# Optimization experiments

Hardware: AMD Instinct MI355X
Metric: run time of the kernel (lower is better)

Reference implementation:

```python
import jax, jax.numpy as jnp
import numpy as np

N_NODES = 50000
N_EDGES = 800000
D_IN = 128
D_OUT = 128


def setup_inputs() -> dict:
    key = jax.random.key(0)
    k1, k2, k3, k4 = jax.random.split(key, 4)
    input_feature = jax.random.normal(k1, (N_NODES, D_IN), dtype=jnp.float32)
    # COO sparse adjacency: edge_index[0]=row (dst), edge_index[1]=col (src)
    edge_index = jax.random.randint(k2, (2, N_EDGES), 0, N_NODES, dtype=jnp.int32)
    edge_weight = jax.random.uniform(k3, (N_EDGES,), dtype=jnp.float32)
    # kaiming-uniform-like init for weight; zeros bias (as in reset_parameters)
    bound = float(np.sqrt(6.0 / D_IN))
    weight = jax.random.uniform(k4, (D_IN, D_OUT), dtype=jnp.float32, minval=-bound, maxval=bound)
    bias = jnp.zeros((D_OUT,), dtype=jnp.float32)
    return {
        "input_feature": input_feature,
        "edge_index": edge_index,
        "edge_weight": edge_weight,
        "weight": weight,
        "bias": bias,
    }


def reference(input_feature, edge_index, edge_weight, weight, bias):
    # support = X @ W  -> [N, D_OUT]
    support = input_feature @ weight
    # sparse A @ support via gather + weighted segment_sum over destination rows
    row, col = edge_index[0], edge_index[1]
    msgs = support[col] * edge_weight[:, None]          # [E, D_OUT]
    output = jax.ops.segment_sum(msgs, row, num_segments=N_NODES)
    return output + bias
```

## Files before the change

### kernel.cpp

```cpp
#include <hip/hip_runtime.h>


#define N_NODES 50000
#define N_EDGES 800000
#define D 128
#define BROWS 66
#define NBUCKET 758
#define SLOT 1536
#define CHUNK 2048
#define EPT 8
#define GEMM_BLOCKS 782
#define PASS1_BLOCKS 391
#define CSTRIDE 16

typedef short bf16x8 __attribute__((ext_vector_type(8)));
typedef float f32x4 __attribute__((ext_vector_type(4)));

__device__ inline unsigned short f2bf(float f) {
    unsigned u = __float_as_uint(f);
    unsigned r = (u + 0x7FFFu + ((u >> 16) & 1u)) >> 16;
    return (unsigned short)r;
}


__global__ __launch_bounds__(256) void wprep_kernel(const float* __restrict__ W,
                                                    unsigned short* __restrict__ WT,
                                                    int* __restrict__ gcursor) {
    int idx = blockIdx.x * 256 + threadIdx.x;
    if (idx < 128 * 128) {
        int k = idx >> 7, n = idx & 127;
        WT[n * 136 + k] = f2bf(W[idx]);
    }
    if (idx < NBUCKET * CSTRIDE) gcursor[idx] = 0;
}

__global__ __launch_bounds__(256) void fused_kernel(const float* __restrict__ X,
                                                    const unsigned short* __restrict__ WT,
                                                    unsigned short* __restrict__ S16,
                                                    const int* __restrict__ ei,
                                                    const float* __restrict__ ew,
                                                    int* __restrict__ gcursor,
                                                    int2* __restrict__ staging) {
    __shared__ __align__(16) char shmem[29712];
    const int t = threadIdx.x;
    const int lane = t & 63, wid = t >> 6;

    if (blockIdx.x < GEMM_BLOCKS) {
        unsigned short* xt = (unsigned short*)shmem;
        const int row0 = blockIdx.x * 64;

        const float4* X4 = (const float4*)X;
#pragma unroll
        for (int i = 0; i < 8; ++i) {
            int idx4 = t + 256 * i;
            int r = idx4 >> 5, c4 = idx4 & 31;
            int gr = row0 + r;
            float4 v = make_float4(0.f, 0.f, 0.f, 0.f);
            if (gr < N_NODES) v = X4[gr * 32 + c4];
            ushort4 u = make_ushort4(f2bf(v.x), f2bf(v.y), f2bf(v.z), f2bf(v.w));
            *(ushort4*)&xt[r * 136 + c4 * 4] = u;
        }
        __syncthreads();

        const int m = lane & 15;
        const int q = lane >> 4;
        const int rbase = wid * 16;

        f32x4 acc[8];
#pragma unroll
        for (int nt = 0; nt < 8; ++nt) acc[nt] = (f32x4){0.f, 0.f, 0.f, 0.f};
#pragma unroll
        for (int ks = 0; ks < 4; ++ks) {
            bf16x8 a = *(const bf16x8*)&xt[(rbase + m) * 136 + ks * 32 + q * 8];
#pragma unroll
            for (int nt = 0; nt < 8; ++nt) {
                bf16x8 b = *(const bf16x8*)&WT[(nt * 16 + m) * 136 + ks * 32 + q * 8];
                acc[nt] = __builtin_amdgcn_mfma_f32_16x16x32_bf16(a, b, acc[nt], 0, 0, 0);
            }
        }
        __syncthreads();
#pragma unroll
        for (int nt = 0; nt < 8; ++nt) {
            int col = nt * 16 + m;
#pragma unroll
            for (int r = 0; r < 4; ++r) {
                int rl = rbase + q * 4 + r;
                xt[rl * 136 + col] = f2bf(acc[nt][r]);
            }
        }
        __syncthreads();
#pragma unroll
        for (int i = 0; i < 4; ++i) {
            int id = t + 256 * i;
            int r = id >> 4, c8 = (id & 15) * 8;
            int gr = row0 + r;
            if (gr < N_NODES)
                *(uint4*)&S16[gr * 128 + c8] = *(const uint4*)&xt[r * 136 + c8];
        }
    } else {
        int* bufx            = (int*)shmem;
        int* bufw            = (int*)(shmem + 8192);
        unsigned short* bof  = (unsigned short*)(shmem + 16384);
        int* hist            = (int*)(shmem + 20480);
        int* lcur            = (int*)(shmem + 23552);
        int* bmg             = (int*)(shmem + 26624);
        int* wsum            = (int*)(shmem + 29696);
        const int base = (blockIdx.x - GEMM_BLOCKS) * CHUNK;

        hist[t] = 0;
        hist[t + 256] = 0;
        hist[t + 512] = 0;
        __syncthreads();

        int rows[EPT];
        int bkt[EPT];
#pragma unroll
        for (int i = 0; i < EPT; ++i) {
            int e = base + t + 256 * i;
            rows[i] = (e < N_EDGES) ? ei[e] : -1;
            bkt[i] = (rows[i] >= 0) ? (rows[i] / BROWS) : -1;
            if (bkt[i] >= 0) atomicAdd(&hist[bkt[i]], 1);
        }
        __syncthreads();

        int run = 0, exv[3], vv[3];
#pragma unroll
        for (int ph = 0; ph < 3; ++ph) {
            int v = hist[ph * 256 + t];
            vv[ph] = v;
            int incl = v;
#pragma unroll
            for (int off = 1; off < 64; off <<= 1) {
                int x = __shfl_up(incl, off, 64);
                if (lane >= off) incl += x;
            }
            if (lane == 63) wsum[wid] = incl;
            __syncthreads();
            int pre = 0, tot = 0;
#pragma unroll
            for (int w = 0; w < 4; ++w) {
                int x = wsum[w];
                if (w < wid) pre += x;
                tot += x;
            }
            exv[ph] = run + incl - v + pre;
            run += tot;
            __syncthreads();
        }
        const int total = run;
        lcur[t] = exv[0];
        lcur[t + 256] = exv[1];
        lcur[t + 512] = exv[2];
#pragma unroll
        for (int ph = 0; ph < 3; ++ph) {
            int b = ph * 256 + t;
            if (b < NBUCKET) {
                int v = vv[ph];
                if (v > 0) {
                    int gb = atomicAdd(&gcursor[b * CSTRIDE], v);
                    bmg[b] = b * SLOT + gb - exv[ph];
                }
            }
        }
        __syncthreads();

#pragma unroll
        for (int i = 0; i < EPT; ++i) {
            if (rows[i] >= 0) {
                int e = base + t + 256 * i;
                int col = ei[N_EDGES + e];
                float w = ew[e];
                int b = bkt[i];
                int lp = atomicAdd(&lcur[b], 1);
                int lrow = rows[i] - b * BROWS;
                bufx[lp] = (int)(((unsigned)lrow << 16) | (unsigned)col);
                bufw[lp] = __float_as_int(w);
                bof[lp] = (unsigned short)b;
            }
        }
        __syncthreads();

        for (int lp = t; lp < total; lp += 256) {
            int b = bof[lp];
            int g = bmg[b] + lp;
            if (g < (b + 1) * SLOT)
                staging[g] = make_int2(bufx[lp], bufw[lp]);
        }
    }
}

__global__ __launch_bounds__(512) void sortgather_kernel(const unsigned short* __restrict__ S16,
                                                         const int* __restrict__ gcursor,
                                                         const int2* __restrict__ staging,
                                                         const float* __restrict__ bias,
                                                         float* __restrict__ out) {
    __shared__ int2 in0[SLOT];
    __shared__ int2 in1[SLOT];
    __shared__ int hist[128];
    __shared__ int exs[128];
    __shared__ int lcur[128];
    __shared__ int wsum[2];
    const int t = threadIdx.x;
    const int b = blockIdx.x;
    const int lane = t & 63;
    int cnt = gcursor[b * CSTRIDE];
    if (cnt > SLOT) cnt = SLOT;

    if (t < 128) hist[t] = 0;
    __syncthreads();

    for (int i = t; i < cnt; i += 512) {
        int2 v = staging[b * SLOT + i];
        in0[i] = v;
        atomicAdd(&hist[((unsigned)v.x >> 16) & 127u], 1);
    }
    __syncthreads();

    int v = 0, incl = 0;
    if (t < 128) {
        v = hist[t];
        incl = v;
#pragma unroll
        for (int off = 1; off < 64; off <<= 1) {
            int x = __shfl_up(incl, off, 64);
            if (lane >= off) incl += x;
        }
        if (lane == 63) wsum[t >> 6] = incl;
    }
    __syncthreads();
    if (t < 128) {
        int pre = (t >= 64) ? wsum[0] : 0;
        int ex = incl - v + pre;
        exs[t] = ex;
        lcur[t] = ex;
    }
    __syncthreads();

    for (int i = t; i < cnt; i += 512) {
        int2 e = in0[i];
        int lr = (int)(((unsigned)e.x >> 16) & 127u);
        int p = atomicAdd(&lcur[lr], 1);
        in1[p] = e;
    }
    __syncthreads();

    const int wv = t >> 6;
    const int sub = lane >> 3;
    const int q = lane & 7;
    const uint4* S4 = (const uint4*)S16;
    const float4* bias4 = (const float4*)bias;
    float4 bb[4];
#pragma unroll
    for (int j = 0; j < 4; ++j) bb[j] = bias4[q * 4 + j];

    for (int rr = wv; rr < BROWS; rr += 8) {
        int beg = exs[rr];
        int end = beg + hist[rr];
        float acc[16];
#pragma unroll
        for (int i = 0; i < 16; ++i) acc[i] = 0.f;
        for (int p = beg + sub; p < end; p += 8) {
            int2 cw = in1[p];
            float w = __int_as_float(cw.y);
            int col = cw.x & 0xFFFF;
            uint4 v0 = S4[col * 16 + q * 2];
            uint4 v1 = S4[col * 16 + q * 2 + 1];
            acc[0]  += __uint_as_float(v0.x << 16) * w;
            acc[1]  += __uint_as_float(v0.x & 0xFFFF0000u) * w;
            acc[2]  += __uint_as_float(v0.y << 16) * w;
            acc[3]  += __uint_as_float(v0.y & 0xFFFF0000u) * w;
            acc[4]  += __uint_as_float(v0.z << 16) * w;
            acc[5]  += __uint_as_float(v0.z & 0xFFFF0000u) * w;
            acc[6]  += __uint_as_float(v0.w << 16) * w;
            acc[7]  += __uint_as_float(v0.w & 0xFFFF0000u) * w;
            acc[8]  += __uint_as_float(v1.x << 16) * w;
            acc[9]  += __uint_as_float(v1.x & 0xFFFF0000u) * w;
            acc[10] += __uint_as_float(v1.y << 16) * w;
            acc[11] += __uint_as_float(v1.y & 0xFFFF0000u) * w;
            acc[12] += __uint_as_float(v1.z << 16) * w;
            acc[13] += __uint_as_float(v1.z & 0xFFFF0000u) * w;
            acc[14] += __uint_as_float(v1.w << 16) * w;
            acc[15] += __uint_as_float(v1.w & 0xFFFF0000u) * w;
        }
#pragma unroll
        for (int i = 0; i < 16; ++i) acc[i] += __shfl_xor(acc[i], 8, 64);
#pragma unroll
        for (int i = 0; i < 16; ++i) acc[i] += __shfl_xor(acc[i], 16, 64);
#pragma unroll
        for (int i = 0; i < 16; ++i) acc[i] += __shfl_xor(acc[i], 32, 64);
        int gr = b * BROWS + rr;
        if (sub == 0 && gr < N_NODES) {
#pragma unroll
            for (int j = 0; j < 4; ++j) {
                float4 o = make_float4(acc[4 * j + 0] + bb[j].x, acc[4 * j + 1] + bb[j].y,
                                       acc[4 * j + 2] + bb[j].z, acc[4 * j + 3] + bb[j].w);
                ((float4*)out)[gr * 32 + q * 4 + j] = o;
            }
        }
    }
}

extern "C" void kernel_launch(void* const* d_in, const int* in_sizes, int n_in,
                              void* d_out, int out_size, void* d_ws, size_t ws_size,
                              hipStream_t stream) {
    const float* X    = (const float*)d_in[0];
    const int*   ei   = (const int*)d_in[1];
    const float* ew   = (const float*)d_in[2];
    const float* W    = (const float*)d_in[3];
    const float* bias = (const float*)d_in[4];
    float* out = (float*)d_out;

    char* ws = (char*)d_ws;
    unsigned short* S16 = (unsigned short*)(ws);
    int2* staging = (int2*)(ws + 12800000);
    int*  gcursor = (int*)(ws + 22114304);
    unsigned short* WT16 = (unsigned short*)(ws + 22162816);

    wprep_kernel<<<64, 256, 0, stream>>>(W, WT16, gcursor);
    fused_kernel<<<GEMM_BLOCKS + PASS1_BLOCKS, 256, 0, stream>>>(X, WT16, S16, ei, ew,
                                                                 gcursor, staging);
    sortgather_kernel<<<NBUCKET, 512, 0, stream>>>(S16, gcursor, staging, bias, out);
}
```

Measured before the change: 148.2 us.

## Reorder to aggregate raw bf16 features first, then apply weight GEMM per bucket

Uses associativity, (A·X)·W instead of A·(X·W). The first kernel now only converts X to bf16, and the gather/segment-sum runs on the converted features. Each bucket then multiplies its aggregated rows by W with MFMA in shared memory before writing fp32 output. This removes the separate GEMM pass and the write and re-read of the support matrix. The costs are a second bf16 rounding of the aggregated values, which can change numerics, and MFMA work padded to 80 rows per bucket. The staging copy into shared memory is also replaced by reading the entries from global memory twice.

Result: no change. 149.5 us (+0.9%).

```diff
diff --git a/kernel.cpp b/kernel.cpp
--- a/kernel.cpp
+++ b/kernel.cpp
@@ -9,7 +9,7 @@
 #define SLOT 1536
 #define CHUNK 2048
 #define EPT 8
-#define GEMM_BLOCKS 782
+#define XCONV_BLOCKS 782
 #define PASS1_BLOCKS 391
 #define CSTRIDE 16
 
@@ -34,68 +34,26 @@
     if (idx < NBUCKET * CSTRIDE) gcursor[idx] = 0;
 }
 
-__global__ __launch_bounds__(256) void fused_kernel(const float* __restrict__ X,
-                                                    const unsigned short* __restrict__ WT,
-                                                    unsigned short* __restrict__ S16,
-                                                    const int* __restrict__ ei,
-                                                    const float* __restrict__ ew,
-                                                    int* __restrict__ gcursor,
-                                                    int2* __restrict__ staging) {
+__global__ __launch_bounds__(256) void prep_kernel(const float* __restrict__ X,
+                                                   unsigned short* __restrict__ X16,
+                                                   const int* __restrict__ ei,
+                                                   const float* __restrict__ ew,
+                                                   int* __restrict__ gcursor,
+                                                   int2* __restrict__ staging) {
     __shared__ __align__(16) char shmem[29712];
     const int t = threadIdx.x;
     const int lane = t & 63, wid = t >> 6;
 
-    if (blockIdx.x < GEMM_BLOCKS) {
-        unsigned short* xt = (unsigned short*)shmem;
-        const int row0 = blockIdx.x * 64;
-
+    if (blockIdx.x < XCONV_BLOCKS) {
         const float4* X4 = (const float4*)X;
 #pragma unroll
         for (int i = 0; i < 8; ++i) {
-            int idx4 = t + 256 * i;
-            int r = idx4 >> 5, c4 = idx4 & 31;
-            int gr = row0 + r;
-            float4 v = make_float4(0.f, 0.f, 0.f, 0.f);
-            if (gr < N_NODES) v = X4[gr * 32 + c4];
-            ushort4 u = make_ushort4(f2bf(v.x), f2bf(v.y), f2bf(v.z), f2bf(v.w));
-            *(ushort4*)&xt[r * 136 + c4 * 4] = u;
-        }
-        __syncthreads();
-
-        const int m = lane & 15;
-        const int q = lane >> 4;
-        const int rbase = wid * 16;
-
-        f32x4 acc[8];
-#pragma unroll
-        for (int nt = 0; nt < 8; ++nt) acc[nt] = (f32x4){0.f, 0.f, 0.f, 0.f};
-#pragma unroll
-        for (int ks = 0; ks < 4; ++ks) {
-            bf16x8 a = *(const bf16x8*)&xt[(rbase + m) * 136 + ks * 32 + q * 8];
-#pragma unroll
-            for (int nt = 0; nt < 8; ++nt) {
-                bf16x8 b = *(const bf16x8*)&WT[(nt * 16 + m) * 136 + ks * 32 + q * 8];
-                acc[nt] = __builtin_amdgcn_mfma_f32_16x16x32_bf16(a, b, acc[nt], 0, 0, 0);
-            }
-        }
-        __syncthreads();
-#pragma unroll
-        for (int nt = 0; nt < 8; ++nt) {
-            int col = nt * 16 + m;
-#pragma unroll
-            for (int r = 0; r < 4; ++r) {
-                int rl = rbase + q * 4 + r;
-                xt[rl * 136 + col] = f2bf(acc[nt][r]);
-            }
-        }
-        __syncthreads();
-#pragma unroll
-        for (int i = 0; i < 4; ++i) {
-            int id = t + 256 * i;
-            int r = id >> 4, c8 = (id & 15) * 8;
-            int gr = row0 + r;
-            if (gr < N_NODES)
-                *(uint4*)&S16[gr * 128 + c8] = *(const uint4*)&xt[r * 136 + c8];
+            int idx4 = blockIdx.x * 2048 + t + 256 * i;
+            if (idx4 < N_NODES * 32) {
+                float4 v = X4[idx4];
+                ((ushort4*)X16)[idx4] =
+                    make_ushort4(f2bf(v.x), f2bf(v.y), f2bf(v.z), f2bf(v.w));
+            }
         }
     } else {
         int* bufx            = (int*)shmem;
@@ -105,7 +63,7 @@
         int* lcur            = (int*)(shmem + 23552);
         int* bmg             = (int*)(shmem + 26624);
         int* wsum            = (int*)(shmem + 29696);
-        const int base = (blockIdx.x - GEMM_BLOCKS) * CHUNK;
+        const int base = (blockIdx.x - XCONV_BLOCKS) * CHUNK;
 
         hist[t] = 0;
         hist[t + 256] = 0;
@@ -189,13 +147,14 @@
     }
 }
 
-__global__ __launch_bounds__(512) void sortgather_kernel(const unsigned short* __restrict__ S16,
-                                                         const int* __restrict__ gcursor,
-                                                         const int2* __restrict__ staging,
-                                                         const float* __restrict__ bias,
-                                                         float* __restrict__ out) {
-    __shared__ int2 in0[SLOT];
+__global__ __launch_bounds__(512) void mega_kernel(const unsigned short* __restrict__ X16,
+                                                   const int* __restrict__ gcursor,
+                                                   const int2* __restrict__ staging,
+                                                   const unsigned short* __restrict__ WT,
+                                                   const float* __restrict__ bias,
+                                                   float* __restrict__ out) {
     __shared__ int2 in1[SLOT];
+    __shared__ unsigned short yt[80 * 136];
     __shared__ int hist[128];
     __shared__ int exs[128];
     __shared__ int lcur[128];
@@ -207,13 +166,11 @@
     if (cnt > SLOT) cnt = SLOT;
 
     if (t < 128) hist[t] = 0;
-    __syncthreads();
-
-    for (int i = t; i < cnt; i += 512) {
-        int2 v = staging[b * SLOT + i];
-        in0[i] = v;
-        atomicAdd(&hist[((unsigned)v.x >> 16) & 127u], 1);
-    }
+    for (int i = t; i < 952; i += 512) ((unsigned*)&yt[66 * 136])[i] = 0u;
+    __syncthreads();
+
+    for (int i = t; i < cnt; i += 512)
+        atomicAdd(&hist[((unsigned)staging[b * SLOT + i].x >> 16) & 127u], 1);
     __syncthreads();
 
     int v = 0, incl = 0;
@@ -237,7 +194,7 @@
     __syncthreads();
 
     for (int i = t; i < cnt; i += 512) {
-        int2 e = in0[i];
+        int2 e = staging[b * SLOT + i];
         int lr = (int)(((unsigned)e.x >> 16) & 127u);
         int p = atomicAdd(&lcur[lr], 1);
         in1[p] = e;
@@ -247,11 +204,7 @@
     const int wv = t >> 6;
     const int sub = lane >> 3;
     const int q = lane & 7;
-    const uint4* S4 = (const uint4*)S16;
-    const float4* bias4 = (const float4*)bias;
-    float4 bb[4];
-#pragma unroll
-    for (int j = 0; j < 4; ++j) bb[j] = bias4[q * 4 + j];
+    const uint4* S4 = (const uint4*)X16;
 
     for (int rr = wv; rr < BROWS; rr += 8) {
         int beg = exs[rr];
@@ -288,14 +241,50 @@
         for (int i = 0; i < 16; ++i) acc[i] += __shfl_xor(acc[i], 16, 64);
 #pragma unroll
         for (int i = 0; i < 16; ++i) acc[i] += __shfl_xor(acc[i], 32, 64);
-        int gr = b * BROWS + rr;
-        if (sub == 0 && gr < N_NODES) {
-#pragma unroll
-            for (int j = 0; j < 4; ++j) {
-                float4 o = make_float4(acc[4 * j + 0] + bb[j].x, acc[4 * j + 1] + bb[j].y,
-                                       acc[4 * j + 2] + bb[j].z, acc[4 * j + 3] + bb[j].w);
-                ((float4*)out)[gr * 32 + q * 4 + j] = o;
-            }
+        if (sub == 0) {
+            ushort4 u0 = make_ushort4(f2bf(acc[0]),  f2bf(acc[1]),
+                                      f2bf(acc[2]),  f2bf(acc[3]));
+            ushort4 u1 = make_ushort4(f2bf(acc[4]),  f2bf(acc[5]),
+                                      f2bf(acc[6]),  f2bf(acc[7]));
+            ushort4 u2 = make_ushort4(f2bf(acc[8]),  f2bf(acc[9]),
+                                      f2bf(acc[10]), f2bf(acc[11]));
+            ushort4 u3 = make_ushort4(f2bf(acc[12]), f2bf(acc[13]),
+                                      f2bf(acc[14]), f2bf(acc[15]));
+            *(ushort4*)&yt[rr * 136 + q * 16]      = u0;
+            *(ushort4*)&yt[rr * 136 + q * 16 + 4]  = u1;
+            *(ushort4*)&yt[rr * 136 + q * 16 + 8]  = u2;
+            *(ushort4*)&yt[rr * 136 + q * 16 + 12] = u3;
+        }
+    }
+    __syncthreads();
+
+    const int m = lane & 15;
+    const int qq = lane >> 4;
+    bf16x8 bfrag[4];
+#pragma unroll
+    for (int ks = 0; ks < 4; ++ks)
+        bfrag[ks] = *(const bf16x8*)&WT[(wv * 16 + m) * 136 + ks * 32 + qq * 8];
+
+    float bv = bias[wv * 16 + m];
+    f32x4 cacc[5];
+#pragma unroll
+    for (int mt = 0; mt < 5; ++mt) cacc[mt] = (f32x4){0.f, 0.f, 0.f, 0.f};
+#pragma unroll
+    for (int mt = 0; mt < 5; ++mt) {
+#pragma unroll
+        for (int ks = 0; ks < 4; ++ks) {
+            bf16x8 a = *(const bf16x8*)&yt[(mt * 16 + m) * 136 + ks * 32 + qq * 8];
+            cacc[mt] = __builtin_amdgcn_mfma_f32_16x16x32_bf16(a, bfrag[ks], cacc[mt], 0, 0, 0);
+        }
+    }
+#pragma unroll
+    for (int mt = 0; mt < 5; ++mt) {
+#pragma unroll
+        for (int r = 0; r < 4; ++r) {
+            int row = mt * 16 + qq * 4 + r;
+            int gr = b * BROWS + row;
+            if (row < BROWS && gr < N_NODES)
+                out[gr * 128 + wv * 16 + m] = cacc[mt][r] + bv;
         }
     }
 }
@@ -311,13 +300,13 @@
     float* out = (float*)d_out;
 
     char* ws = (char*)d_ws;
-    unsigned short* S16 = (unsigned short*)(ws);
+    unsigned short* X16 = (unsigned short*)(ws);
     int2* staging = (int2*)(ws + 12800000);
     int*  gcursor = (int*)(ws + 22114304);
     unsigned short* WT16 = (unsigned short*)(ws + 22162816);
 
     wprep_kernel<<<64, 256, 0, stream>>>(W, WT16, gcursor);
-    fused_kernel<<<GEMM_BLOCKS + PASS1_BLOCKS, 256, 0, stream>>>(X, WT16, S16, ei, ew,
+    prep_kernel<<<XCONV_BLOCKS + PASS1_BLOCKS, 256, 0, stream>>>(X, X16, ei, ew,
                                                                  gcursor, staging);
-    sortgather_kernel<<<NBUCKET, 512, 0, stream>>>(S16, gcursor, staging, bias, out);
-}
+    mega_kernel<<<NBUCKET, 512, 0, stream>>>(X16, gcursor, staging, WT16, bias, out);
+}
```
